# Kernel optimization log

Hardware: AMD Instinct MI355X
Metric: run time of the kernel (lower is better)

## Reference

```python
import jax, jax.numpy as jnp
import numpy as np

B, S, T = 32, 64, 64      # batch, encoder len, max_seq_length (decode steps)
H, E, V = 512, 512, 32000  # hidden, embedding, vocab


def setup_inputs() -> dict:
    key = jax.random.key(0)
    ks = jax.random.split(key, 10)
    sc = 1.0 / np.sqrt(H)
    return {
        "encoder_outputs": jax.random.normal(ks[0], (B, S, H), jnp.float32),
        "encoder_hidden": jax.random.normal(ks[1], (1, B, H), jnp.float32),
        "emb": jax.random.normal(ks[2], (V, E), jnp.float32) * 0.02,
        "Wa_w": jax.random.normal(ks[3], (H, H), jnp.float32) * sc,
        "Wa_b": jnp.zeros((H,), jnp.float32),
        "Ua_w": jax.random.normal(ks[4], (H, H), jnp.float32) * sc,
        "Ua_b": jnp.zeros((H,), jnp.float32),
        "Va_w": jax.random.normal(ks[5], (1, H), jnp.float32) * sc,
        "Va_b": jnp.zeros((1,), jnp.float32),
        "W_ih": jax.random.normal(ks[6], (3 * H, E + H), jnp.float32) * sc,
        "W_hh": jax.random.normal(ks[7], (3 * H, H), jnp.float32) * sc,
        "b_ih": jnp.zeros((3 * H,), jnp.float32),
        "b_hh": jnp.zeros((3 * H,), jnp.float32),
        "out_w": jax.random.normal(ks[8], (V, H), jnp.float32) * sc,
        "out_b": jnp.zeros((V,), jnp.float32),
        "sos_token": 1,
    }


def _decode(encoder_outputs, encoder_hidden, emb, Wa_w, Wa_b, Ua_w, Ua_b,
            Va_w, Va_b, W_ih, W_hh, b_ih, b_hh, out_w, out_b, sos_token):
    # Ua(keys) is loop-invariant; hoist it (same math as per-step recompute).
    keys_proj = jnp.einsum('bsh,gh->bsg', encoder_outputs, Ua_w) + Ua_b  # [B,S,H]

    def step(carry, _):
        h, tok = carry                      # h: [B,H], tok: [B] (greedy, detached)
        x = emb[tok]                        # [B,E] embedding lookup (eval: no dropout)
        # Bahdanau attention: Va(tanh(Wa(q) + Ua(k)))
        q = h @ Wa_w.T + Wa_b               # [B,H]
        scores = jnp.einsum('bsh,h->bs', jnp.tanh(q[:, None, :] + keys_proj), Va_w[0]) + Va_b[0]
        w = jax.nn.softmax(scores, axis=-1)                     # [B,S]
        context = jnp.einsum('bs,bsh->bh', w, encoder_outputs)  # [B,H]
        # PyTorch GRU cell (gate order r,z,n)
        gi = jnp.concatenate([x, context], axis=-1) @ W_ih.T + b_ih  # [B,3H]
        gh = h @ W_hh.T + b_hh                                        # [B,3H]
        gi_r, gi_z, gi_n = jnp.split(gi, 3, axis=-1)
        gh_r, gh_z, gh_n = jnp.split(gh, 3, axis=-1)
        r = jax.nn.sigmoid(gi_r + gh_r)
        z = jax.nn.sigmoid(gi_z + gh_z)
        n = jnp.tanh(gi_n + r * gh_n)
        h_new = (1.0 - z) * n + z * h       # [B,H]
        logits = h_new @ out_w.T + out_b    # [B,V]
        tok_new = jnp.argmax(logits, axis=-1)  # greedy feedback (topk(1))
        return (h_new, tok_new), (logits, w)

    h0 = encoder_hidden[0]
    tok0 = jnp.full((B,), sos_token, dtype=jnp.int32)
    (h_last, _), (logits, attn) = jax.lax.scan(step, (h0, tok0), None, length=T)
    logprobs = jax.nn.log_softmax(jnp.transpose(logits, (1, 0, 2)), axis=-1)  # [B,T,V]
    return logprobs, h_last[None], jnp.transpose(attn, (1, 0, 2))


def reference(encoder_outputs, encoder_hidden, emb, Wa_w, Wa_b, Ua_w, Ua_b,
              Va_w, Va_b, W_ih, W_hh, b_ih, b_hh, out_w, out_b, sos_token):
    return _decode(encoder_outputs, encoder_hidden, emb, Wa_w, Wa_b, Ua_w, Ua_b,
                   Va_w, Va_b, W_ih, W_hh, b_ih, b_hh, out_w, out_b, sos_token)
```

## Files before the change

### kernel.cpp

```cpp
#include <hip/hip_runtime.h>

#define Bn 32
#define Sn 64
#define Tn 64
#define Hn 512
#define Vn 32000

#define KP_OFF   0u
#define H0_OFF   1048576u
#define H1_OFF   1064960u
#define CTX_OFF  1081344u
#define PK_OFF   1097728u
#define TOK_OFF  1101824u
#define DONE_OFF 1101856u

__global__ void __launch_bounds__(256) kp_kernel(const float* __restrict__ enc,
                                                 const float* __restrict__ Ua_w,
                                                 const float* __restrict__ Ua_b,
                                                 float* __restrict__ kp) {
  __shared__ __align__(16) float ea[32][68];
  __shared__ __align__(16) float ua[64][68];
  const int tid = threadIdx.x;
  const int bs0 = blockIdx.x * 32, g0 = blockIdx.y * 64;
  const int g_l = tid & 63;
  const int wv  = tid >> 6;
  float acc[8];
#pragma unroll
  for (int r = 0; r < 8; r++) acc[r] = 0.f;
  for (int kc = 0; kc < 8; kc++) {
    const int k0 = kc * 64;
#pragma unroll
    for (int r = 0; r < 8; r++) { int f = tid + r * 256; int b = f >> 6, k = f & 63;
      ea[b][k] = enc[(bs0 + b) * Hn + k0 + k]; }
#pragma unroll
    for (int r = 0; r < 16; r++) { int f = tid + r * 256; int g = f >> 6, k = f & 63;
      ua[g][k] = Ua_w[(g0 + g) * Hn + k0 + k]; }
    __syncthreads();
#pragma unroll
    for (int kk = 0; kk < 16; kk++) {
      float4 u4 = *(const float4*)&ua[g_l][kk * 4];
#pragma unroll
      for (int r = 0; r < 8; r++) {
        int bs_l = wv + 4 * r;
        float4 e4 = *(const float4*)&ea[bs_l][kk * 4];
        acc[r] += u4.x * e4.x + u4.y * e4.y + u4.z * e4.z + u4.w * e4.w;
      }
    }
    __syncthreads();
  }
  const float bias = Ua_b[g0 + g_l];
#pragma unroll
  for (int r = 0; r < 8; r++) {
    int bs = bs0 + wv + 4 * r;
    kp[bs * Hn + g0 + g_l] = acc[r] + bias;
  }
}

__global__ void __launch_bounds__(256) init_kernel(const float* __restrict__ eh,
                                                   const int* __restrict__ sos,
                                                   float* __restrict__ h0,
                                                   unsigned long long* __restrict__ packed,
                                                   int* __restrict__ tok,
                                                   unsigned int* __restrict__ done) {
  const int tid = threadIdx.x;
  for (int i = tid; i < Bn * Hn; i += 256) h0[i] = eh[i];
  if (tid < Bn) tok[tid] = sos[0];
  for (int i = tid; i < Tn * Bn; i += 256) packed[i] = 0ull;
  if (tid < Tn) done[tid] = 0u;
}

__global__ void __launch_bounds__(256) attn_kernel(const float* __restrict__ enc,
                                                   const float* __restrict__ kp,
                                                   const float* __restrict__ Wa_w,
                                                   const float* __restrict__ Wa_b,
                                                   const float* __restrict__ Va_w,
                                                   const float* __restrict__ Va_b,
                                                   const float* __restrict__ h_cur,
                                                   float* __restrict__ ctx,
                                                   float* __restrict__ attn_out,
                                                   int t) {
  __shared__ __align__(16) float hb[Hn];
  __shared__ __align__(16) float qb[Hn];
  __shared__ __align__(16) float va[Hn];
  __shared__ float sp[64][4];
  __shared__ float wgt[64];
  const int b = blockIdx.x, tid = threadIdx.x;
  for (int i = tid; i < Hn; i += 256) { hb[i] = h_cur[b * Hn + i]; va[i] = Va_w[i]; }
  __syncthreads();
#pragma unroll
  for (int rr = 0; rr < 2; rr++) {
    const int r = tid + rr * 256;
    const float4* wrow = (const float4*)&Wa_w[r * Hn];
    float a = 0.f;
    for (int k4 = 0; k4 < Hn / 4; k4++) {
      float4 w4 = wrow[k4];
      float4 h4 = *(const float4*)&hb[k4 * 4];
      a += w4.x * h4.x + w4.y * h4.y + w4.z * h4.z + w4.w * h4.w;
    }
    qb[r] = a + Wa_b[r];
  }
  __syncthreads();
  {
    const int s = tid >> 2, j = tid & 3;
    const float4* kp4 = (const float4*)&kp[(b * Sn + s) * Hn + j * 128];
    const float4* q4p = (const float4*)&qb[j * 128];
    const float4* v4p = (const float4*)&va[j * 128];
    float a = 0.f;
#pragma unroll 8
    for (int k4 = 0; k4 < 32; k4++) {
      float4 kv = kp4[k4];
      float4 q4 = q4p[k4];
      float4 v4 = v4p[k4];
      a += tanhf(q4.x + kv.x) * v4.x;
      a += tanhf(q4.y + kv.y) * v4.y;
      a += tanhf(q4.z + kv.z) * v4.z;
      a += tanhf(q4.w + kv.w) * v4.w;
    }
    sp[s][j] = a;
  }
  __syncthreads();
  if (tid < 64) {
    float v = sp[tid][0] + sp[tid][1] + sp[tid][2] + sp[tid][3] + Va_b[0];
    float m = v;
    for (int off = 32; off; off >>= 1) m = fmaxf(m, __shfl_xor(m, off));
    float e = expf(v - m);
    float ssum = e;
    for (int off = 32; off; off >>= 1) ssum += __shfl_xor(ssum, off);
    float w = e / ssum;
    wgt[tid] = w;
    attn_out[(b * Tn + t) * Sn + tid] = w;
  }
  __syncthreads();
#pragma unroll
  for (int rr = 0; rr < 2; rr++) {
    const int g = tid + rr * 256;
    float a = 0.f;
    for (int s = 0; s < Sn; s++) a += wgt[s] * enc[(b * Sn + s) * Hn + g];
    ctx[b * Hn + g] = a;
  }
}

__global__ void __launch_bounds__(256) gru_kernel(const float* __restrict__ emb,
                                                  const int* __restrict__ tok,
                                                  const float* __restrict__ ctx,
                                                  const float* __restrict__ h_cur,
                                                  const float* __restrict__ W_ih,
                                                  const float* __restrict__ W_hh,
                                                  const float* __restrict__ b_ih,
                                                  const float* __restrict__ b_hh,
                                                  float* __restrict__ h_nxt) {
  __shared__ __align__(16) float ch[16][132];
  __shared__ int tks[16];
  const int tid = threadIdx.x;
  const int b_l = tid & 15, i_l = tid >> 4;
  const int i0 = blockIdx.x * 16, b0 = blockIdx.y * 16;
  const int ig = i0 + i_l;
  const int b  = b0 + b_l;
  if (tid < 16) tks[tid] = tok[b0 + tid];
  __syncthreads();
  float air = 0, aiz = 0, ain = 0, ahr = 0, ahz = 0, ahn = 0;
  const float4* wr_r = (const float4*)&W_ih[(ig)          * 1024];
  const float4* wr_z = (const float4*)&W_ih[(ig + 512)    * 1024];
  const float4* wr_n = (const float4*)&W_ih[(ig + 1024)   * 1024];
  for (int c = 0; c < 4; c++) {
    const int k0 = c * 128;
#pragma unroll
    for (int r = 0; r < 8; r++) { int f = tid + r * 256; int bb = f >> 7, kk = f & 127;
      ch[bb][kk] = emb[tks[bb] * Hn + k0 + kk]; }
    __syncthreads();
#pragma unroll
    for (int k4 = 0; k4 < 32; k4++) {
      float4 x4 = *(const float4*)&ch[b_l][k4 * 4];
      float4 w;
      w = wr_r[(k0 >> 2) + k4]; air += w.x * x4.x + w.y * x4.y + w.z * x4.z + w.w * x4.w;
      w = wr_z[(k0 >> 2) + k4]; aiz += w.x * x4.x + w.y * x4.y + w.z * x4.z + w.w * x4.w;
      w = wr_n[(k0 >> 2) + k4]; ain += w.x * x4.x + w.y * x4.y + w.z * x4.z + w.w * x4.w;
    }
    __syncthreads();
  }
  for (int c = 0; c < 4; c++) {
    const int k0 = c * 128;
#pragma unroll
    for (int r = 0; r < 8; r++) { int f = tid + r * 256; int bb = f >> 7, kk = f & 127;
      ch[bb][kk] = ctx[(b0 + bb) * Hn + k0 + kk]; }
    __syncthreads();
#pragma unroll
    for (int k4 = 0; k4 < 32; k4++) {
      float4 x4 = *(const float4*)&ch[b_l][k4 * 4];
      float4 w;
      w = wr_r[128 + (k0 >> 2) + k4]; air += w.x * x4.x + w.y * x4.y + w.z * x4.z + w.w * x4.w;
      w = wr_z[128 + (k0 >> 2) + k4]; aiz += w.x * x4.x + w.y * x4.y + w.z * x4.z + w.w * x4.w;
      w = wr_n[128 + (k0 >> 2) + k4]; ain += w.x * x4.x + w.y * x4.y + w.z * x4.z + w.w * x4.w;
    }
    __syncthreads();
  }
  const float4* hr_r = (const float4*)&W_hh[(ig)        * Hn];
  const float4* hr_z = (const float4*)&W_hh[(ig + 512)  * Hn];
  const float4* hr_n = (const float4*)&W_hh[(ig + 1024) * Hn];
  for (int c = 0; c < 4; c++) {
    const int k0 = c * 128;
#pragma unroll
    for (int r = 0; r < 8; r++) { int f = tid + r * 256; int bb = f >> 7, kk = f & 127;
      ch[bb][kk] = h_cur[(b0 + bb) * Hn + k0 + kk]; }
    __syncthreads();
#pragma unroll
    for (int k4 = 0; k4 < 32; k4++) {
      float4 x4 = *(const float4*)&ch[b_l][k4 * 4];
      float4 w;
      w = hr_r[(k0 >> 2) + k4]; ahr += w.x * x4.x + w.y * x4.y + w.z * x4.z + w.w * x4.w;
      w = hr_z[(k0 >> 2) + k4]; ahz += w.x * x4.x + w.y * x4.y + w.z * x4.z + w.w * x4.w;
      w = hr_n[(k0 >> 2) + k4]; ahn += w.x * x4.x + w.y * x4.y + w.z * x4.z + w.w * x4.w;
    }
    __syncthreads();
  }
  const float hv = h_cur[b * Hn + ig];
  const float r = 1.f / (1.f + expf(-(air + b_ih[ig] + ahr + b_hh[ig])));
  const float z = 1.f / (1.f + expf(-(aiz + b_ih[512 + ig] + ahz + b_hh[512 + ig])));
  const float n = tanhf(ain + b_ih[1024 + ig] + r * (ahn + b_hh[1024 + ig]));
  h_nxt[b * Hn + ig] = (1.f - z) * n + z * hv;
}

__global__ void __launch_bounds__(256) logits_kernel(const float* __restrict__ h_new,
                                                     const float* __restrict__ out_w,
                                                     const float* __restrict__ out_b,
                                                     float* __restrict__ logits_out,
                                                     unsigned long long* __restrict__ packed,
                                                     int* __restrict__ tok,
                                                     unsigned int* __restrict__ done,
                                                     int t) {
  __shared__ __align__(16) float hc[32][516];
  __shared__ float redm[32][33];
  __shared__ int   redi[32][33];
  __shared__ unsigned int rank;
  const int tid = threadIdx.x;
  const int vg = tid >> 3;
  const int bg = tid & 7;
  const int v0 = blockIdx.x * 64;
  for (int f = tid; f < Bn * (Hn / 4); f += 256) {
    int bb = f >> 7, kk = f & 127;
    *(float4*)&hc[bb][kk * 4] = *(const float4*)&h_new[bb * Hn + kk * 4];
  }
  __syncthreads();
  float acc[2][4];
#pragma unroll
  for (int j = 0; j < 2; j++)
#pragma unroll
    for (int i = 0; i < 4; i++) acc[j][i] = 0.f;
  const float* wbase = out_w + (size_t)(v0 + vg * 2) * Hn;
#pragma unroll 8
  for (int k4 = 0; k4 < 128; k4++) {
    float4 w0 = *(const float4*)(wbase + 0 * Hn + k4 * 4);
    float4 w1 = *(const float4*)(wbase + 1 * Hn + k4 * 4);
#pragma unroll
    for (int i = 0; i < 4; i++) {
      float4 h4 = *(const float4*)&hc[bg + 8 * i][k4 * 4];
      acc[0][i] += w0.x * h4.x + w0.y * h4.y + w0.z * h4.z + w0.w * h4.w;
      acc[1][i] += w1.x * h4.x + w1.y * h4.y + w1.z * h4.z + w1.w * h4.w;
    }
  }
  float bias[2];
#pragma unroll
  for (int j = 0; j < 2; j++) bias[j] = out_b[v0 + vg * 2 + j];
#pragma unroll
  for (int i = 0; i < 4; i++) {
    const int b = bg + 8 * i;
    float best = -1e38f; int bidx = v0;
#pragma unroll
    for (int j = 0; j < 2; j++) {
      float x = acc[j][i] + bias[j];
      logits_out[((size_t)b * Tn + t) * Vn + v0 + vg * 2 + j] = x;
      if (x > best) { best = x; bidx = v0 + vg * 2 + j; }
    }
    redm[b][vg] = best; redi[b][vg] = bidx;
  }
  __syncthreads();
  if (tid < 32) {
    const int b = tid;
    float best = redm[b][0]; int bidx = redi[b][0];
    for (int g = 1; g < 32; g++)
      if (redm[b][g] > best) { best = redm[b][g]; bidx = redi[b][g]; }
    unsigned int u = __float_as_uint(best);
    unsigned int key = (u & 0x80000000u) ? ~u : (u | 0x80000000u);
    unsigned long long pk = ((unsigned long long)key << 32) |
                            (unsigned long long)(0xFFFFFFFFu - (unsigned int)bidx);
    atomicMax(&packed[t * Bn + b], pk);
  }
  __threadfence();
  if (tid == 0) rank = atomicAdd(&done[t], 1u);
  __syncthreads();
  if (rank == gridDim.x - 1) {
    __threadfence();
    if (tid < 32) {
      unsigned long long pk = atomicAdd(&packed[t * Bn + tid], 0ull);
      tok[tid] = (int)(0xFFFFFFFFu - (unsigned int)(pk & 0xFFFFFFFFull));
    }
  }
}

__global__ void __launch_bounds__(256) finalize_kernel(float* __restrict__ out1,
                                                       const float* __restrict__ h_src,
                                                       float* __restrict__ out2) {
  if (blockIdx.x == (unsigned)(Bn * Tn)) {
    for (int i = threadIdx.x; i < Bn * Hn; i += 256) out2[i] = h_src[i];
    return;
  }
  float* row = out1 + (size_t)blockIdx.x * Vn;
  const int tid = threadIdx.x;
  __shared__ float red[4];
  const float4* r4 = (const float4*)row;
  float m = -1e38f;
  for (int i = tid; i < Vn / 4; i += 256) {
    float4 v = r4[i];
    m = fmaxf(m, fmaxf(fmaxf(v.x, v.y), fmaxf(v.z, v.w)));
  }
  for (int off = 32; off; off >>= 1) m = fmaxf(m, __shfl_xor(m, off));
  if ((tid & 63) == 0) red[tid >> 6] = m;
  __syncthreads();
  m = fmaxf(fmaxf(red[0], red[1]), fmaxf(red[2], red[3]));
  __syncthreads();
  float s = 0.f;
  for (int i = tid; i < Vn / 4; i += 256) {
    float4 v = r4[i];
    s += __expf(v.x - m) + __expf(v.y - m) + __expf(v.z - m) + __expf(v.w - m);
  }
  for (int off = 32; off; off >>= 1) s += __shfl_xor(s, off);
  if ((tid & 63) == 0) red[tid >> 6] = s;
  __syncthreads();
  s = red[0] + red[1] + red[2] + red[3];
  const float lz = m + logf(s);
  float4* w4p = (float4*)row;
  for (int i = tid; i < Vn / 4; i += 256) {
    float4 v = r4[i];
    v.x -= lz; v.y -= lz; v.z -= lz; v.w -= lz;
    w4p[i] = v;
  }
}

extern "C" void kernel_launch(void* const* d_in, const int* in_sizes, int n_in,
                              void* d_out, int out_size, void* d_ws, size_t ws_size,
                              hipStream_t stream) {
  (void)in_sizes; (void)n_in; (void)out_size; (void)ws_size;
  const float* enc   = (const float*)d_in[0];
  const float* ehid  = (const float*)d_in[1];
  const float* emb   = (const float*)d_in[2];
  const float* Wa_w  = (const float*)d_in[3];
  const float* Wa_b  = (const float*)d_in[4];
  const float* Ua_w  = (const float*)d_in[5];
  const float* Ua_b  = (const float*)d_in[6];
  const float* Va_w  = (const float*)d_in[7];
  const float* Va_b  = (const float*)d_in[8];
  const float* W_ih  = (const float*)d_in[9];
  const float* W_hh  = (const float*)d_in[10];
  const float* b_ih  = (const float*)d_in[11];
  const float* b_hh  = (const float*)d_in[12];
  const float* out_w = (const float*)d_in[13];
  const float* out_b = (const float*)d_in[14];
  const int*   sos   = (const int*)d_in[15];

  float* ws    = (float*)d_ws;
  float* kp    = ws + KP_OFF;
  float* hbuf0 = ws + H0_OFF;
  float* hbuf1 = ws + H1_OFF;
  float* ctx   = ws + CTX_OFF;
  unsigned long long* packed = (unsigned long long*)(ws + PK_OFF);
  int*          tok  = (int*)(ws + TOK_OFF);
  unsigned int* done = (unsigned int*)(ws + DONE_OFF);

  float* out1 = (float*)d_out;
  float* out2 = out1 + (size_t)Bn * Tn * Vn;
  float* out3 = out2 + Bn * Hn;

  kp_kernel<<<dim3(64, 8), 256, 0, stream>>>(enc, Ua_w, Ua_b, kp);
  init_kernel<<<1, 256, 0, stream>>>(ehid, sos, hbuf0, packed, tok, done);
  for (int t = 0; t < Tn; t++) {
    float* h_cur = (t & 1) ? hbuf1 : hbuf0;
    float* h_nxt = (t & 1) ? hbuf0 : hbuf1;
    attn_kernel<<<Bn, 256, 0, stream>>>(enc, kp, Wa_w, Wa_b, Va_w, Va_b, h_cur, ctx, out3, t);
    gru_kernel<<<dim3(32, 2), 256, 0, stream>>>(emb, tok, ctx, h_cur, W_ih, W_hh, b_ih, b_hh, h_nxt);
    logits_kernel<<<500, 256, 0, stream>>>(h_nxt, out_w, out_b, out1, packed, tok, done, t);
  }
  finalize_kernel<<<Bn * Tn + 1, 256, 0, stream>>>(out1, hbuf0, out2);
}
```

Baseline: 13.65 ms.

## Fuse per-step attention, GRU and logits kernels into one ticketed step kernel

Replaces the three per-step launches with a single 596-block kernel. Each block takes a ticket from an atomic counter, and the ticket assigns it a role: attention, GRU or logits. Roles wait on release-counter flags, so GRU work that does not depend on the context (embedding and hidden-state matvecs) overlaps with attention, and logits blocks warm out_w into cache while they wait. This removes two launches and kernel boundaries per step, plus the separate token-writing pass, since GRU reads argmax results straight from the packed buffer. The cost is spin-waits that rely on the producer blocks being scheduled first; the ticket order is meant to guarantee this, but it is fragile with respect to occupancy.

```diff
diff --git a/kernel.cpp b/kernel.cpp
--- a/kernel.cpp
+++ b/kernel.cpp
@@ -11,8 +11,14 @@
 #define H1_OFF   1064960u
 #define CTX_OFF  1081344u
 #define PK_OFF   1097728u
-#define TOK_OFF  1101824u
-#define DONE_OFF 1101856u
+#define CTL_OFF  1101824u
+
+__device__ __forceinline__ float agl(const float* p) {
+  return __hip_atomic_load(p, __ATOMIC_RELAXED, __HIP_MEMORY_SCOPE_AGENT);
+}
+__device__ __forceinline__ void ags(float* p, float v) {
+  __hip_atomic_store(p, v, __ATOMIC_RELAXED, __HIP_MEMORY_SCOPE_AGENT);
+}
 
 __global__ void __launch_bounds__(256) kp_kernel(const float* __restrict__ enc,
                                                  const float* __restrict__ Ua_w,
@@ -57,242 +63,261 @@
 }
 
 __global__ void __launch_bounds__(256) init_kernel(const float* __restrict__ eh,
-                                                   const int* __restrict__ sos,
                                                    float* __restrict__ h0,
                                                    unsigned long long* __restrict__ packed,
-                                                   int* __restrict__ tok,
-                                                   unsigned int* __restrict__ done) {
+                                                   unsigned int* __restrict__ ctl) {
   const int tid = threadIdx.x;
   for (int i = tid; i < Bn * Hn; i += 256) h0[i] = eh[i];
-  if (tid < Bn) tok[tid] = sos[0];
   for (int i = tid; i < Tn * Bn; i += 256) packed[i] = 0ull;
-  if (tid < Tn) done[tid] = 0u;
-}
-
-__global__ void __launch_bounds__(256) attn_kernel(const float* __restrict__ enc,
-                                                   const float* __restrict__ kp,
-                                                   const float* __restrict__ Wa_w,
-                                                   const float* __restrict__ Wa_b,
-                                                   const float* __restrict__ Va_w,
-                                                   const float* __restrict__ Va_b,
-                                                   const float* __restrict__ h_cur,
-                                                   float* __restrict__ ctx,
-                                                   float* __restrict__ attn_out,
-                                                   int t) {
-  __shared__ __align__(16) float hb[Hn];
-  __shared__ __align__(16) float qb[Hn];
-  __shared__ __align__(16) float va[Hn];
-  __shared__ float sp[64][4];
-  __shared__ float wgt[64];
-  const int b = blockIdx.x, tid = threadIdx.x;
-  for (int i = tid; i < Hn; i += 256) { hb[i] = h_cur[b * Hn + i]; va[i] = Va_w[i]; }
+  if (tid < Tn) ctl[tid] = 0u;
+}
+
+__global__ void __launch_bounds__(256, 2) step_kernel(
+    const float* __restrict__ enc, const float* __restrict__ kp,
+    const float* __restrict__ Wa_w, const float* __restrict__ Wa_b,
+    const float* __restrict__ Va_w, const float* __restrict__ Va_b,
+    const float* __restrict__ emb, const float* __restrict__ W_ih,
+    const float* __restrict__ W_hh, const float* __restrict__ b_ih,
+    const float* __restrict__ b_hh, const float* __restrict__ out_w,
+    const float* __restrict__ out_b, const int* __restrict__ sos,
+    const float* __restrict__ h_cur, float* __restrict__ h_nxt,
+    float* __restrict__ ctx, unsigned long long* __restrict__ packed,
+    unsigned int* __restrict__ ctl,
+    float* __restrict__ logits_out, float* __restrict__ attn_out, int t) {
+  __shared__ __align__(16) char smem[74496];
+  __shared__ unsigned int s_tk;
+  const int tid = threadIdx.x;
+  if (tid == 0)
+    s_tk = __hip_atomic_fetch_add(&ctl[t], 1u, __ATOMIC_RELAXED,
+                                  __HIP_MEMORY_SCOPE_AGENT) & 0xFFFFu;
   __syncthreads();
-#pragma unroll
-  for (int rr = 0; rr < 2; rr++) {
-    const int r = tid + rr * 256;
-    const float4* wrow = (const float4*)&Wa_w[r * Hn];
-    float a = 0.f;
-    for (int k4 = 0; k4 < Hn / 4; k4++) {
-      float4 w4 = wrow[k4];
-      float4 h4 = *(const float4*)&hb[k4 * 4];
-      a += w4.x * h4.x + w4.y * h4.y + w4.z * h4.z + w4.w * h4.w;
-    }
-    qb[r] = a + Wa_b[r];
-  }
-  __syncthreads();
-  {
-    const int s = tid >> 2, j = tid & 3;
-    const float4* kp4 = (const float4*)&kp[(b * Sn + s) * Hn + j * 128];
-    const float4* q4p = (const float4*)&qb[j * 128];
-    const float4* v4p = (const float4*)&va[j * 128];
-    float a = 0.f;
+  const unsigned int tk = s_tk;
+
+  if (tk < 32u) {
+    const int b = (int)tk;
+    float* hb  = (float*)smem;
+    float* qb  = hb + Hn;
+    float* va  = qb + Hn;
+    float* sp  = va + Hn;
+    float* wgt = sp + 256;
+    for (int i = tid; i < Hn; i += 256) { hb[i] = h_cur[b * Hn + i]; va[i] = Va_w[i]; }
+    __syncthreads();
+#pragma unroll
+    for (int rr = 0; rr < 2; rr++) {
+      const int r = tid + rr * 256;
+      const float4* wrow = (const float4*)&Wa_w[r * Hn];
+      float a = 0.f;
+      for (int k4 = 0; k4 < Hn / 4; k4++) {
+        float4 w4 = wrow[k4];
+        float4 h4 = *(const float4*)&hb[k4 * 4];
+        a += w4.x * h4.x + w4.y * h4.y + w4.z * h4.z + w4.w * h4.w;
+      }
+      qb[r] = a + Wa_b[r];
+    }
+    __syncthreads();
+    {
+      const int s = tid >> 2, j = tid & 3;
+      const float4* kp4 = (const float4*)&kp[(b * Sn + s) * Hn + j * 128];
+      const float4* q4p = (const float4*)&qb[j * 128];
+      const float4* v4p = (const float4*)&va[j * 128];
+      float a = 0.f;
 #pragma unroll 8
-    for (int k4 = 0; k4 < 32; k4++) {
-      float4 kv = kp4[k4];
-      float4 q4 = q4p[k4];
-      float4 v4 = v4p[k4];
-      a += tanhf(q4.x + kv.x) * v4.x;
-      a += tanhf(q4.y + kv.y) * v4.y;
-      a += tanhf(q4.z + kv.z) * v4.z;
-      a += tanhf(q4.w + kv.w) * v4.w;
-    }
-    sp[s][j] = a;
-  }
-  __syncthreads();
-  if (tid < 64) {
-    float v = sp[tid][0] + sp[tid][1] + sp[tid][2] + sp[tid][3] + Va_b[0];
-    float m = v;
-    for (int off = 32; off; off >>= 1) m = fmaxf(m, __shfl_xor(m, off));
-    float e = expf(v - m);
-    float ssum = e;
-    for (int off = 32; off; off >>= 1) ssum += __shfl_xor(ssum, off);
-    float w = e / ssum;
-    wgt[tid] = w;
-    attn_out[(b * Tn + t) * Sn + tid] = w;
-  }
-  __syncthreads();
-#pragma unroll
-  for (int rr = 0; rr < 2; rr++) {
-    const int g = tid + rr * 256;
-    float a = 0.f;
-    for (int s = 0; s < Sn; s++) a += wgt[s] * enc[(b * Sn + s) * Hn + g];
-    ctx[b * Hn + g] = a;
-  }
-}
-
-__global__ void __launch_bounds__(256) gru_kernel(const float* __restrict__ emb,
-                                                  const int* __restrict__ tok,
-                                                  const float* __restrict__ ctx,
-                                                  const float* __restrict__ h_cur,
-                                                  const float* __restrict__ W_ih,
-                                                  const float* __restrict__ W_hh,
-                                                  const float* __restrict__ b_ih,
-                                                  const float* __restrict__ b_hh,
-                                                  float* __restrict__ h_nxt) {
-  __shared__ __align__(16) float ch[16][132];
-  __shared__ int tks[16];
-  const int tid = threadIdx.x;
-  const int b_l = tid & 15, i_l = tid >> 4;
-  const int i0 = blockIdx.x * 16, b0 = blockIdx.y * 16;
-  const int ig = i0 + i_l;
-  const int b  = b0 + b_l;
-  if (tid < 16) tks[tid] = tok[b0 + tid];
-  __syncthreads();
-  float air = 0, aiz = 0, ain = 0, ahr = 0, ahz = 0, ahn = 0;
-  const float4* wr_r = (const float4*)&W_ih[(ig)          * 1024];
-  const float4* wr_z = (const float4*)&W_ih[(ig + 512)    * 1024];
-  const float4* wr_n = (const float4*)&W_ih[(ig + 1024)   * 1024];
-  for (int c = 0; c < 4; c++) {
-    const int k0 = c * 128;
-#pragma unroll
-    for (int r = 0; r < 8; r++) { int f = tid + r * 256; int bb = f >> 7, kk = f & 127;
-      ch[bb][kk] = emb[tks[bb] * Hn + k0 + kk]; }
-    __syncthreads();
-#pragma unroll
-    for (int k4 = 0; k4 < 32; k4++) {
-      float4 x4 = *(const float4*)&ch[b_l][k4 * 4];
-      float4 w;
-      w = wr_r[(k0 >> 2) + k4]; air += w.x * x4.x + w.y * x4.y + w.z * x4.z + w.w * x4.w;
-      w = wr_z[(k0 >> 2) + k4]; aiz += w.x * x4.x + w.y * x4.y + w.z * x4.z + w.w * x4.w;
-      w = wr_n[(k0 >> 2) + k4]; ain += w.x * x4.x + w.y * x4.y + w.z * x4.z + w.w * x4.w;
-    }
-    __syncthreads();
-  }
-  for (int c = 0; c < 4; c++) {
-    const int k0 = c * 128;
-#pragma unroll
-    for (int r = 0; r < 8; r++) { int f = tid + r * 256; int bb = f >> 7, kk = f & 127;
-      ch[bb][kk] = ctx[(b0 + bb) * Hn + k0 + kk]; }
-    __syncthreads();
-#pragma unroll
-    for (int k4 = 0; k4 < 32; k4++) {
-      float4 x4 = *(const float4*)&ch[b_l][k4 * 4];
-      float4 w;
-      w = wr_r[128 + (k0 >> 2) + k4]; air += w.x * x4.x + w.y * x4.y + w.z * x4.z + w.w * x4.w;
-      w = wr_z[128 + (k0 >> 2) + k4]; aiz += w.x * x4.x + w.y * x4.y + w.z * x4.z + w.w * x4.w;
-      w = wr_n[128 + (k0 >> 2) + k4]; ain += w.x * x4.x + w.y * x4.y + w.z * x4.z + w.w * x4.w;
-    }
-    __syncthreads();
-  }
-  const float4* hr_r = (const float4*)&W_hh[(ig)        * Hn];
-  const float4* hr_z = (const float4*)&W_hh[(ig + 512)  * Hn];
-  const float4* hr_n = (const float4*)&W_hh[(ig + 1024) * Hn];
-  for (int c = 0; c < 4; c++) {
-    const int k0 = c * 128;
-#pragma unroll
-    for (int r = 0; r < 8; r++) { int f = tid + r * 256; int bb = f >> 7, kk = f & 127;
-      ch[bb][kk] = h_cur[(b0 + bb) * Hn + k0 + kk]; }
-    __syncthreads();
-#pragma unroll
-    for (int k4 = 0; k4 < 32; k4++) {
-      float4 x4 = *(const float4*)&ch[b_l][k4 * 4];
-      float4 w;
-      w = hr_r[(k0 >> 2) + k4]; ahr += w.x * x4.x + w.y * x4.y + w.z * x4.z + w.w * x4.w;
-      w = hr_z[(k0 >> 2) + k4]; ahz += w.x * x4.x + w.y * x4.y + w.z * x4.z + w.w * x4.w;
-      w = hr_n[(k0 >> 2) + k4]; ahn += w.x * x4.x + w.y * x4.y + w.z * x4.z + w.w * x4.w;
-    }
-    __syncthreads();
-  }
-  const float hv = h_cur[b * Hn + ig];
-  const float r = 1.f / (1.f + expf(-(air + b_ih[ig] + ahr + b_hh[ig])));
-  const float z = 1.f / (1.f + expf(-(aiz + b_ih[512 + ig] + ahz + b_hh[512 + ig])));
-  const float n = tanhf(ain + b_ih[1024 + ig] + r * (ahn + b_hh[1024 + ig]));
-  h_nxt[b * Hn + ig] = (1.f - z) * n + z * hv;
-}
-
-__global__ void __launch_bounds__(256) logits_kernel(const float* __restrict__ h_new,
-                                                     const float* __restrict__ out_w,
-                                                     const float* __restrict__ out_b,
-                                                     float* __restrict__ logits_out,
-                                                     unsigned long long* __restrict__ packed,
-                                                     int* __restrict__ tok,
-                                                     unsigned int* __restrict__ done,
-                                                     int t) {
-  __shared__ __align__(16) float hc[32][516];
-  __shared__ float redm[32][33];
-  __shared__ int   redi[32][33];
-  __shared__ unsigned int rank;
-  const int tid = threadIdx.x;
-  const int vg = tid >> 3;
-  const int bg = tid & 7;
-  const int v0 = blockIdx.x * 64;
-  for (int f = tid; f < Bn * (Hn / 4); f += 256) {
-    int bb = f >> 7, kk = f & 127;
-    *(float4*)&hc[bb][kk * 4] = *(const float4*)&h_new[bb * Hn + kk * 4];
-  }
-  __syncthreads();
-  float acc[2][4];
-#pragma unroll
-  for (int j = 0; j < 2; j++)
-#pragma unroll
-    for (int i = 0; i < 4; i++) acc[j][i] = 0.f;
-  const float* wbase = out_w + (size_t)(v0 + vg * 2) * Hn;
+      for (int k4 = 0; k4 < 32; k4++) {
+        float4 kv = kp4[k4];
+        float4 q4 = q4p[k4];
+        float4 v4 = v4p[k4];
+        a += tanhf(q4.x + kv.x) * v4.x;
+        a += tanhf(q4.y + kv.y) * v4.y;
+        a += tanhf(q4.z + kv.z) * v4.z;
+        a += tanhf(q4.w + kv.w) * v4.w;
+      }
+      sp[s * 4 + j] = a;
+    }
+    __syncthreads();
+    if (tid < 64) {
+      float v = sp[tid * 4 + 0] + sp[tid * 4 + 1] + sp[tid * 4 + 2] + sp[tid * 4 + 3] + Va_b[0];
+      float m = v;
+      for (int off = 32; off; off >>= 1) m = fmaxf(m, __shfl_xor(m, off));
+      float e = expf(v - m);
+      float ssum = e;
+      for (int off = 32; off; off >>= 1) ssum += __shfl_xor(ssum, off);
+      float w = e / ssum;
+      wgt[tid] = w;
+      attn_out[(b * Tn + t) * Sn + tid] = w;
+    }
+    __syncthreads();
+#pragma unroll
+    for (int rr = 0; rr < 2; rr++) {
+      const int g = tid + rr * 256;
+      float a = 0.f;
+      for (int s = 0; s < Sn; s++) a += wgt[s] * enc[(b * Sn + s) * Hn + g];
+      ags(&ctx[b * Hn + g], a);
+    }
+    __syncthreads();
+    if (tid == 0)
+      __hip_atomic_fetch_add(&ctl[t], 1u << 16, __ATOMIC_RELEASE, __HIP_MEMORY_SCOPE_AGENT);
+
+  } else if (tk < 96u) {
+    const int g = (int)tk - 32;
+    const int b_l = tid & 15, i_l = tid >> 4;
+    const int i0 = (g & 31) * 16, b0 = (g >> 5) * 16;
+    const int ig = i0 + i_l;
+    const int b  = b0 + b_l;
+    float* ch = (float*)smem;
+    int* tks  = (int*)(ch + 16 * 132);
+    if (tid < 16) {
+      int tkn;
+      if (t == 0) {
+        tkn = sos[0];
+      } else {
+        unsigned long long pk = __hip_atomic_load(&packed[(t - 1) * Bn + b0 + tid],
+                                                  __ATOMIC_RELAXED, __HIP_MEMORY_SCOPE_AGENT);
+        tkn = (int)(0xFFFFFFFFu - (unsigned int)(pk & 0xFFFFFFFFull));
+      }
+      tks[tid] = tkn;
+    }
+    __syncthreads();
+    float air = 0, aiz = 0, ain = 0, ahr = 0, ahz = 0, ahn = 0;
+    const float4* wr_r = (const float4*)&W_ih[(size_t)(ig)        * 1024];
+    const float4* wr_z = (const float4*)&W_ih[(size_t)(ig + 512)  * 1024];
+    const float4* wr_n = (const float4*)&W_ih[(size_t)(ig + 1024) * 1024];
+    for (int c = 0; c < 4; c++) {
+      const int k0 = c * 128;
+#pragma unroll
+      for (int r = 0; r < 8; r++) { int f = tid + r * 256; int bb = f >> 7, kk = f & 127;
+        ch[bb * 132 + kk] = emb[(size_t)tks[bb] * Hn + k0 + kk]; }
+      __syncthreads();
+#pragma unroll
+      for (int k4 = 0; k4 < 32; k4++) {
+        float4 x4 = *(const float4*)&ch[b_l * 132 + k4 * 4];
+        float4 w;
+        w = wr_r[(k0 >> 2) + k4]; air += w.x * x4.x + w.y * x4.y + w.z * x4.z + w.w * x4.w;
+        w = wr_z[(k0 >> 2) + k4]; aiz += w.x * x4.x + w.y * x4.y + w.z * x4.z + w.w * x4.w;
+        w = wr_n[(k0 >> 2) + k4]; ain += w.x * x4.x + w.y * x4.y + w.z * x4.z + w.w * x4.w;
+      }
+      __syncthreads();
+    }
+    const float4* hr_r = (const float4*)&W_hh[(size_t)(ig)        * Hn];
+    const float4* hr_z = (const float4*)&W_hh[(size_t)(ig + 512)  * Hn];
+    const float4* hr_n = (const float4*)&W_hh[(size_t)(ig + 1024) * Hn];
+    for (int c = 0; c < 4; c++) {
+      const int k0 = c * 128;
+#pragma unroll
+      for (int r = 0; r < 8; r++) { int f = tid + r * 256; int bb = f >> 7, kk = f & 127;
+        ch[bb * 132 + kk] = h_cur[(b0 + bb) * Hn + k0 + kk]; }
+      __syncthreads();
+#pragma unroll
+      for (int k4 = 0; k4 < 32; k4++) {
+        float4 x4 = *(const float4*)&ch[b_l * 132 + k4 * 4];
+        float4 w;
+        w = hr_r[(k0 >> 2) + k4]; ahr += w.x * x4.x + w.y * x4.y + w.z * x4.z + w.w * x4.w;
+        w = hr_z[(k0 >> 2) + k4]; ahz += w.x * x4.x + w.y * x4.y + w.z * x4.z + w.w * x4.w;
+        w = hr_n[(k0 >> 2) + k4]; ahn += w.x * x4.x + w.y * x4.y + w.z * x4.z + w.w * x4.w;
+      }
+      __syncthreads();
+    }
+    if (tid == 0) {
+      while (((__hip_atomic_load(&ctl[t], __ATOMIC_RELAXED, __HIP_MEMORY_SCOPE_AGENT) >> 16) & 0xFFu) < 32u)
+        __builtin_amdgcn_s_sleep(8);
+    }
+    __syncthreads();
+    asm volatile("" ::: "memory");
+    for (int c = 0; c < 4; c++) {
+      const int k0 = c * 128;
+#pragma unroll
+      for (int r = 0; r < 8; r++) { int f = tid + r * 256; int bb = f >> 7, kk = f & 127;
+        ch[bb * 132 + kk] = agl(&ctx[(b0 + bb) * Hn + k0 + kk]); }
+      __syncthreads();
+#pragma unroll
+      for (int k4 = 0; k4 < 32; k4++) {
+        float4 x4 = *(const float4*)&ch[b_l * 132 + k4 * 4];
+        float4 w;
+        w = wr_r[128 + (k0 >> 2) + k4]; air += w.x * x4.x + w.y * x4.y + w.z * x4.z + w.w * x4.w;
+        w = wr_z[128 + (k0 >> 2) + k4]; aiz += w.x * x4.x + w.y * x4.y + w.z * x4.z + w.w * x4.w;
+        w = wr_n[128 + (k0 >> 2) + k4]; ain += w.x * x4.x + w.y * x4.y + w.z * x4.z + w.w * x4.w;
+      }
+      __syncthreads();
+    }
+    const float hv = h_cur[b * Hn + ig];
+    const float r = 1.f / (1.f + expf(-(air + b_ih[ig] + ahr + b_hh[ig])));
+    const float z = 1.f / (1.f + expf(-(aiz + b_ih[512 + ig] + ahz + b_hh[512 + ig])));
+    const float n = tanhf(ain + b_ih[1024 + ig] + r * (ahn + b_hh[1024 + ig]));
+    ags(&h_nxt[b * Hn + ig], (1.f - z) * n + z * hv);
+    __syncthreads();
+    if (tid == 0)
+      __hip_atomic_fetch_add(&ctl[t], 1u << 24, __ATOMIC_RELEASE, __HIP_MEMORY_SCOPE_AGENT);
+
+  } else {
+    const int v0 = ((int)tk - 96) * 64;
+    float* hc   = (float*)smem;
+    float* redm = hc + 32 * 516;
+    int*   redi = (int*)(redm + 32 * 33);
+    const int vg = tid >> 3;
+    const int bg = tid & 7;
+    bool ready = ((__hip_atomic_load(&ctl[t], __ATOMIC_RELAXED, __HIP_MEMORY_SCOPE_AGENT) >> 24) >= 64u);
+    if (!ready) {
+      const float4* wb4 = (const float4*)(out_w + (size_t)v0 * Hn);
+      float d = 0.f;
+      for (int f = tid; f < 64 * 128; f += 256) {
+        float4 v = wb4[f];
+        d += v.x + v.y + v.z + v.w;
+      }
+      asm volatile("" :: "v"(d));
+    }
+    if (tid == 0) {
+      while ((__hip_atomic_load(&ctl[t], __ATOMIC_RELAXED, __HIP_MEMORY_SCOPE_AGENT) >> 24) < 64u)
+        __builtin_amdgcn_s_sleep(8);
+    }
+    __syncthreads();
+    asm volatile("" ::: "memory");
+    for (int f = tid; f < Bn * Hn; f += 256) {
+      int bb = f >> 9, kk = f & 511;
+      hc[bb * 516 + kk] = agl(&h_nxt[f]);
+    }
+    __syncthreads();
+    float acc[2][4];
+#pragma unroll
+    for (int j = 0; j < 2; j++)
+#pragma unroll
+      for (int i = 0; i < 4; i++) acc[j][i] = 0.f;
+    const float* wbase = out_w + (size_t)(v0 + vg * 2) * Hn;
 #pragma unroll 8
-  for (int k4 = 0; k4 < 128; k4++) {
-    float4 w0 = *(const float4*)(wbase + 0 * Hn + k4 * 4);
-    float4 w1 = *(const float4*)(wbase + 1 * Hn + k4 * 4);
+    for (int k4 = 0; k4 < 128; k4++) {
+      float4 w0 = *(const float4*)(wbase + 0 * Hn + k4 * 4);
+      float4 w1 = *(const float4*)(wbase + 1 * Hn + k4 * 4);
+#pragma unroll
+      for (int i = 0; i < 4; i++) {
+        float4 h4 = *(const float4*)&hc[(bg + 8 * i) * 516 + k4 * 4];
+        acc[0][i] += w0.x * h4.x + w0.y * h4.y + w0.z * h4.z + w0.w * h4.w;
+        acc[1][i] += w1.x * h4.x + w1.y * h4.y + w1.z * h4.z + w1.w * h4.w;
+      }
+    }
+    float bias[2];
+#pragma unroll
+    for (int j = 0; j < 2; j++) bias[j] = out_b[v0 + vg * 2 + j];
 #pragma unroll
     for (int i = 0; i < 4; i++) {
-      float4 h4 = *(const float4*)&hc[bg + 8 * i][k4 * 4];
-      acc[0][i] += w0.x * h4.x + w0.y * h4.y + w0.z * h4.z + w0.w * h4.w;
-      acc[1][i] += w1.x * h4.x + w1.y * h4.y + w1.z * h4.z + w1.w * h4.w;
-    }
-  }
-  float bias[2];
-#pragma unroll
-  for (int j = 0; j < 2; j++) bias[j] = out_b[v0 + vg * 2 + j];
-#pragma unroll
-  for (int i = 0; i < 4; i++) {
-    const int b = bg + 8 * i;
-    float best = -1e38f; int bidx = v0;
-#pragma unroll
-    for (int j = 0; j < 2; j++) {
-      float x = acc[j][i] + bias[j];
-      logits_out[((size_t)b * Tn + t) * Vn + v0 + vg * 2 + j] = x;
-      if (x > best) { best = x; bidx = v0 + vg * 2 + j; }
-    }
-    redm[b][vg] = best; redi[b][vg] = bidx;
-  }
-  __syncthreads();
-  if (tid < 32) {
-    const int b = tid;
-    float best = redm[b][0]; int bidx = redi[b][0];
-    for (int g = 1; g < 32; g++)
-      if (redm[b][g] > best) { best = redm[b][g]; bidx = redi[b][g]; }
-    unsigned int u = __float_as_uint(best);
-    unsigned int key = (u & 0x80000000u) ? ~u : (u | 0x80000000u);
-    unsigned long long pk = ((unsigned long long)key << 32) |
-                            (unsigned long long)(0xFFFFFFFFu - (unsigned int)bidx);
-    atomicMax(&packed[t * Bn + b], pk);
-  }
-  __threadfence();
-  if (tid == 0) rank = atomicAdd(&done[t], 1u);
-  __syncthreads();
-  if (rank == gridDim.x - 1) {
-    __threadfence();
+      const int b = bg + 8 * i;
+      float best = -1e38f; int bidx = v0;
+#pragma unroll
+      for (int j = 0; j < 2; j++) {
+        float x = acc[j][i] + bias[j];
+        __builtin_nontemporal_store(x, &logits_out[((size_t)b * Tn + t) * Vn + v0 + vg * 2 + j]);
+        if (x > best) { best = x; bidx = v0 + vg * 2 + j; }
+      }
+      redm[b * 33 + vg] = best; redi[b * 33 + vg] = bidx;
+    }
+    __syncthreads();
     if (tid < 32) {
-      unsigned long long pk = atomicAdd(&packed[t * Bn + tid], 0ull);
-      tok[tid] = (int)(0xFFFFFFFFu - (unsigned int)(pk & 0xFFFFFFFFull));
+      const int b = tid;
+      float best = redm[b * 33 + 0]; int bidx = redi[b * 33 + 0];
+      for (int g2 = 1; g2 < 32; g2++)
+        if (redm[b * 33 + g2] > best) { best = redm[b * 33 + g2]; bidx = redi[b * 33 + g2]; }
+      unsigned int u = __float_as_uint(best);
+      unsigned int key = (u & 0x80000000u) ? ~u : (u | 0x80000000u);
+      unsigned long long pk = ((unsigned long long)key << 32) |
+                              (unsigned long long)(0xFFFFFFFFu - (unsigned int)bidx);
+      atomicMax(&packed[t * Bn + b], pk);
     }
   }
 }
@@ -363,21 +388,22 @@
   float* hbuf1 = ws + H1_OFF;
   float* ctx   = ws + CTX_OFF;
   unsigned long long* packed = (unsigned long long*)(ws + PK_OFF);
-  int*          tok  = (int*)(ws + TOK_OFF);
-  unsigned int* done = (unsigned int*)(ws + DONE_OFF);
+  unsigned int* ctl = (unsigned int*)(ws + CTL_OFF);
 
   float* out1 = (float*)d_out;
   float* out2 = out1 + (size_t)Bn * Tn * Vn;
   float* out3 = out2 + Bn * Hn;
 
   kp_kernel<<<dim3(64, 8), 256, 0, stream>>>(enc, Ua_w, Ua_b, kp);
-  init_kernel<<<1, 256, 0, stream>>>(ehid, sos, hbuf0, packed, tok, done);
+  init_kernel<<<1, 256, 0, stream>>>(ehid, hbuf0, packed, ctl);
   for (int t = 0; t < Tn; t++) {
     float* h_cur = (t & 1) ? hbuf1 : hbuf0;
     float* h_nxt = (t & 1) ? hbuf0 : hbuf1;
-    attn_kernel<<<Bn, 256, 0, stream>>>(enc, kp, Wa_w, Wa_b, Va_w, Va_b, h_cur, ctx, out3, t);
-    gru_kernel<<<dim3(32, 2), 256, 0, stream>>>(emb, tok, ctx, h_cur, W_ih, W_hh, b_ih, b_hh, h_nxt);
-    logits_kernel<<<500, 256, 0, stream>>>(h_nxt, out_w, out_b, out1, packed, tok, done, t);
+    step_kernel<<<596, 256, 0, stream>>>(enc, kp, Wa_w, Wa_b, Va_w, Va_b,
+                                         emb, W_ih, W_hh, b_ih, b_hh,
+                                         out_w, out_b, sos,
+                                         h_cur, h_nxt, ctx, packed, ctl,
+                                         out1, out3, t);
   }
   finalize_kernel<<<Bn * Tn + 1, 256, 0, stream>>>(out1, hbuf0, out2);
 }
```

Measured after the change: 11.01 ms. -19.3%, faster.
